# Kernel tuning notes

Hardware: AMD Instinct MI355X
Metric: run time of the kernel (lower is better)

The kernel has to match this reference:

```python
import jax, jax.numpy as jnp
import numpy as np

N, IN_CH, OUT_CH = 2, 16, 32
SPATIAL = (20, 20, 20, 20)
KER = (3, 3, 3, 3)


def setup_inputs() -> dict:
    key = jax.random.key(0)
    kx, kw = jax.random.split(key)
    x = jax.random.normal(kx, (N, IN_CH) + SPATIAL, dtype=jnp.float32)
    # kaiming-uniform-like init scale; exact init distribution irrelevant for correctness baseline
    fan_in = IN_CH * int(np.prod(KER))
    bound = float(np.sqrt(6.0 / fan_in))
    w = jax.random.uniform(kw, (IN_CH, OUT_CH) + KER, dtype=jnp.float32,
                           minval=-bound, maxval=bound)
    return {"x": x, "w": w}


def reference(x, w):
    # x: [n, in_ch, d1, d2, d3, d4]; w: [in_ch, out_ch, k1, k2, k3, k4]
    # valid 4D convolution (cross-correlation), stride 1 -- same math as the
    # torch as_strided im2col + tensordot, but expressed as a sum over the
    # (small, fixed) kernel offsets to avoid materializing the im2col tensor.
    kd = w.shape[2:]
    od = tuple(x.shape[2 + i] - kd[i] + 1 for i in range(4))  # output spatial dims
    out = jnp.zeros((x.shape[0], w.shape[1]) + od, dtype=x.dtype)
    for a in range(kd[0]):
        for b in range(kd[1]):
            for c in range(kd[2]):
                for d in range(kd[3]):
                    patch = x[:, :, a:a + od[0], b:b + od[1], c:c + od[2], d:d + od[3]]
                    out = out + jnp.einsum('ncijkl,co->noijkl', patch, w[:, :, a, b, c, d])
    return out
```

## Files before the change

kernel.cpp:

```cpp
#include <hip/hip_runtime.h>


typedef unsigned short ushort_t;
typedef __attribute__((ext_vector_type(8)))  __bf16 bf16x8;
typedef __attribute__((ext_vector_type(16))) float  f32x16;
typedef __attribute__((ext_vector_type(4)))  unsigned int uint4v;

__device__ __forceinline__ ushort_t f2bf(float f) {
    union { float f; unsigned int u; } v; v.f = f;
    unsigned int r = v.u + 0x7FFFu + ((v.u >> 16) & 1u);
    return (ushort_t)(r >> 16);
}

__global__ __launch_bounds__(256) void prepass(const float* __restrict__ x,
                                               const float* __restrict__ w,
                                               ushort_t* __restrict__ xt,
                                               ushort_t* __restrict__ wt) {
    const int blk = blockIdx.x;
    if (blk < 1250) {
        const int g = blk * 256 + threadIdx.x;
        const int n = g / 160000, rem = g % 160000;
        const float* xs = x + (size_t)n * 2560000 + rem;
        unsigned int pk[8];
        #pragma unroll
        for (int e = 0; e < 8; ++e) {
            unsigned int lo = f2bf(xs[(size_t)(2 * e) * 160000]);
            unsigned int hi = f2bf(xs[(size_t)(2 * e + 1) * 160000]);
            pk[e] = lo | (hi << 16);
        }
        uint4v* q = (uint4v*)xt + (size_t)g * 2;
        uint4v q0; q0[0] = pk[0]; q0[1] = pk[1]; q0[2] = pk[2]; q0[3] = pk[3];
        uint4v q1; q1[0] = pk[4]; q1[1] = pk[5]; q1[2] = pk[6]; q1[3] = pk[7];
        q[0] = q0; q[1] = q1;
    } else {
        const int s = (blk - 1250) * 256 + threadIdx.x;
        if (s < 41472) {
            const int ic = s / 2592, rem = s % 2592;
            const int oc = rem / 81, tap = rem % 81;
            wt[tap * 512 + oc * 16 + ic] = f2bf(w[s]);
        }
    }
}

__global__ __launch_bounds__(256, 4) void conv4d_mfma(
    const ushort_t* __restrict__ xt, const ushort_t* __restrict__ wt,
    float* __restrict__ out)
{
    const int wgid = blockIdx.x;
    const int g = (wgid & 7) * 243 + (wgid >> 3);
    const int n = g / 972;
    int rem = g - n * 972;
    const int j = rem / 54;  rem -= j * 54;
    const int i = rem / 3;
    const int q = rem - i * 3;

    const int t = threadIdx.x;
    const int lane = t & 63, wv = t >> 6;
    const int col = lane & 31, ic8 = lane >> 5;

    const int T = q * 4 + wv;
    const int sp = T * 30 + col;
    const int spc = sp > 359 ? 359 : sp;
    const int cb = spc * 32 + ic8 * 16;

    f32x16 acc0, acc1, acc2;
    #pragma unroll
    for (int r = 0; r < 16; ++r) { acc0[r] = 0.0f; acc1[r] = 0.0f; acc2[r] = 0.0f; }

    const char* xnij = (const char*)(xt + (size_t)n * 2560000
                                        + (size_t)i * 128000 + (size_t)j * 6400);

    #pragma unroll 3
    for (int ab = 0; ab < 9; ++ab) {
        const int a = ab / 3, b = ab % 3;
        const char* xs = xnij + ((size_t)a * 128000 + (size_t)b * 6400) * 2;
        const ushort_t* wtb = wt + (size_t)ab * 4608 + col * 16 + ic8 * 8;
        #pragma unroll
        for (int c = 0; c < 3; ++c) {
            bf16x8 af0 = *(const bf16x8*)(wtb + (c * 3 + 0) * 512);
            bf16x8 af1 = *(const bf16x8*)(wtb + (c * 3 + 1) * 512);
            bf16x8 af2 = *(const bf16x8*)(wtb + (c * 3 + 2) * 512);
            bf16x8 bv  = *(const bf16x8*)(xs + cb + c * 640);
            acc0 = __builtin_amdgcn_mfma_f32_32x32x16_bf16(af0, bv, acc0, 0, 0, 0);
            acc1 = __builtin_amdgcn_mfma_f32_32x32x16_bf16(af1, bv, acc1, 0, 0, 0);
            acc2 = __builtin_amdgcn_mfma_f32_32x32x16_bf16(af2, bv, acc2, 0, 0, 0);
        }
    }

    const int s = sp;
    const int k = s / 20, ls = s % 20;
    const bool val = (col <= 29) && (ls <= 17) && (s <= 357);
    float* po = out + (size_t)n * 3359232 + (size_t)i * 5832 + (size_t)j * 324
                    + (size_t)ic8 * 419904 + k * 18 + ls;
    const int src1 = (lane & 32) | ((col + 1) & 31);
    const int src2 = (lane & 32) | ((col + 2) & 31);

    #pragma unroll
    for (int r = 0; r < 16; ++r) {
        const float v1 = __shfl(acc1[r], src1, 64);
        const float v2 = __shfl(acc2[r], src2, 64);
        const float res = acc0[r] + v1 + v2;
        const int offr = ((r & 3) + 8 * (r >> 2)) * 104976;
        if (val) po[offr] = res;
    }
}

extern "C" void kernel_launch(void* const* d_in, const int* in_sizes, int n_in,
                              void* d_out, int out_size, void* d_ws, size_t ws_size,
                              hipStream_t stream) {
    const float* x = (const float*)d_in[0];
    const float* w = (const float*)d_in[1];
    float* out = (float*)d_out;

    ushort_t* xt = (ushort_t*)d_ws;
    ushort_t* wt = (ushort_t*)((char*)d_ws + (size_t)10240000);

    prepass<<<dim3(1412), 256, 0, stream>>>(x, w, xt, wt);
    conv4d_mfma<<<dim3(1944), 256, 0, stream>>>(xt, wt, out);
}
```

Measured before the change: 46.45 us.

## Stage weight tiles in LDS via double-buffered global_load_lds

Weight fragments were previously read straight from global memory by every wave. Now each (a,b) weight slab is copied into a double-buffered LDS array with async global_load_lds, and the next slab is prefetched while the current one feeds the MFMAs. The prepass weight layout is split by ic half so each 16-byte LDS chunk lines up with the direct-to-LDS copy. This adds a __syncthreads per iteration and about 18 KB of LDS per block, and it drops the unroll-3 pragma, which may reduce overlap and occupancy.

```diff
diff --git a/kernel.cpp b/kernel.cpp
--- a/kernel.cpp
+++ b/kernel.cpp
@@ -10,6 +10,12 @@
     union { float f; unsigned int u; } v; v.f = f;
     unsigned int r = v.u + 0x7FFFu + ((v.u >> 16) & 1u);
     return (ushort_t)(r >> 16);
+}
+
+__device__ __forceinline__ void gload16(const ushort_t* g, ushort_t* l) {
+    __builtin_amdgcn_global_load_lds(
+        (const __attribute__((address_space(1))) unsigned int*)g,
+        (__attribute__((address_space(3))) unsigned int*)l, 16, 0, 0);
 }
 
 __global__ __launch_bounds__(256) void prepass(const float* __restrict__ x,
@@ -37,7 +43,7 @@
         if (s < 41472) {
             const int ic = s / 2592, rem = s % 2592;
             const int oc = rem / 81, tap = rem % 81;
-            wt[tap * 512 + oc * 16 + ic] = f2bf(w[s]);
+            wt[tap * 512 + (ic >> 3) * 256 + oc * 8 + (ic & 7)] = f2bf(w[s]);
         }
     }
 }
@@ -46,6 +52,8 @@
     const ushort_t* __restrict__ xt, const ushort_t* __restrict__ wt,
     float* __restrict__ out)
 {
+    __shared__ ushort_t lwt[2][4608];
+
     const int wgid = blockIdx.x;
     const int g = (wgid & 7) * 243 + (wgid >> 3);
     const int n = g / 972;
@@ -62,6 +70,7 @@
     const int sp = T * 30 + col;
     const int spc = sp > 359 ? 359 : sp;
     const int cb = spc * 32 + ic8 * 16;
+    const int aoffB = ic8 * 512 + col * 16;
 
     f32x16 acc0, acc1, acc2;
     #pragma unroll
@@ -70,16 +79,32 @@
     const char* xnij = (const char*)(xt + (size_t)n * 2560000
                                         + (size_t)i * 128000 + (size_t)j * 6400);
 
-    #pragma unroll 3
+    {
+        const ushort_t* gw = wt;
+        gload16(gw + t * 8,        lwt[0] + (wv << 9));
+        gload16(gw + 2048 + t * 8, lwt[0] + 2048 + (wv << 9));
+        if (t < 64) gload16(gw + 4096 + t * 8, lwt[0] + 4096);
+    }
+
     for (int ab = 0; ab < 9; ++ab) {
+        __syncthreads();
+
+        if (ab < 8) {
+            const ushort_t* gw = wt + (size_t)(ab + 1) * 4608;
+            ushort_t* lw = lwt[(ab + 1) & 1];
+            gload16(gw + t * 8,        lw + (wv << 9));
+            gload16(gw + 2048 + t * 8, lw + 2048 + (wv << 9));
+            if (t < 64) gload16(gw + 4096 + t * 8, lw + 4096);
+        }
+
         const int a = ab / 3, b = ab % 3;
         const char* xs = xnij + ((size_t)a * 128000 + (size_t)b * 6400) * 2;
-        const ushort_t* wtb = wt + (size_t)ab * 4608 + col * 16 + ic8 * 8;
+        const char* wbase = (const char*)lwt[ab & 1];
         #pragma unroll
         for (int c = 0; c < 3; ++c) {
-            bf16x8 af0 = *(const bf16x8*)(wtb + (c * 3 + 0) * 512);
-            bf16x8 af1 = *(const bf16x8*)(wtb + (c * 3 + 1) * 512);
-            bf16x8 af2 = *(const bf16x8*)(wtb + (c * 3 + 2) * 512);
+            bf16x8 af0 = *(const bf16x8*)(wbase + (c * 3 + 0) * 1024 + aoffB);
+            bf16x8 af1 = *(const bf16x8*)(wbase + (c * 3 + 1) * 1024 + aoffB);
+            bf16x8 af2 = *(const bf16x8*)(wbase + (c * 3 + 2) * 1024 + aoffB);
             bf16x8 bv  = *(const bf16x8*)(xs + cb + c * 640);
             acc0 = __builtin_amdgcn_mfma_f32_32x32x16_bf16(af0, bv, acc0, 0, 0, 0);
             acc1 = __builtin_amdgcn_mfma_f32_32x32x16_bf16(af1, bv, acc1, 0, 0, 0);
```

New measurement: 40.84 us. -12.1%, faster.
